# Performance work log

Hardware: AMD Instinct MI355X
Metric: run time of the kernel (lower is better)

Reference implementation:

```python
import jax, jax.numpy as jnp
import numpy as np


def fps(xyz, nsamples):
    # xyz: [B, N, 3] -> [B, nsamples] furthest-point-sample indices (int32)
    def single(p):
        N = p.shape[0]
        def step(carry, _):
            dists, last = carry
            d = jnp.sum((p - p[last]) ** 2, axis=-1)
            dists = jnp.minimum(dists, d)
            return (dists, jnp.argmax(dists).astype(jnp.int32)), last
        init = (jnp.full((N,), 1e10, p.dtype), jnp.int32(0))
        _, idx = jax.lax.scan(step, init, None, length=nsamples)
        return idx
    return jax.vmap(single)(xyz)


def bn_relu(x, g, b, m, v):
    # inference BatchNorm2d folded into scale/shift, then ReLU; x: [B,C,S,N]
    s = g * jax.lax.rsqrt(v + 1e-5)
    return jax.nn.relu(x * s[None, :, None, None] + (b - m * s)[None, :, None, None])


def setup_inputs() -> dict:
    key = jax.random.key(0)
    ks = jax.random.split(key, 6)
    B, N, C, S = 8, 16384, 64, 5
    return dict(
        fg_xyz=jax.random.normal(ks[0], (B, N, 3), jnp.float32),
        fg_features=jax.random.normal(ks[1], (B, C, N), jnp.float32),
        bg_xyz=jax.random.normal(ks[2], (B, N, 3), jnp.float32),
        bg_features=jax.random.normal(ks[3], (B, C, N), jnp.float32),
        w1=jax.random.normal(ks[4], (C, 2 * C), jnp.float32) * (1.0 / np.sqrt(2 * C)),
        g1=jnp.ones((C,), jnp.float32), b1=jnp.zeros((C,), jnp.float32),
        m1=jnp.zeros((C,), jnp.float32), v1=jnp.ones((C,), jnp.float32),
        w2=jax.random.normal(ks[5], (C, C), jnp.float32) * (1.0 / np.sqrt(C)),
        g2=jnp.ones((C,), jnp.float32), b2=jnp.zeros((C,), jnp.float32),
        m2=jnp.zeros((C,), jnp.float32), v2=jnp.ones((C,), jnp.float32),
        nsamples=5,
    )


def reference(fg_xyz, fg_features, bg_xyz, bg_features,
              w1, g1, b1, m1, v1, w2, g2, b2, m2, v2, nsamples):
    B, C, N = fg_features.shape
    S = nsamples
    # D-FPS sample S background points, gather their features: [B, C, S]
    idx = fps(bg_xyz, S)
    sample_bg = jnp.take_along_axis(
        bg_features, jnp.broadcast_to(idx[:, None, :], (B, C, S)), axis=2)
    fg_exp = fg_features[:, :, None, :]                           # [B, C, 1, N]
    # candidates = [fg itself, S sampled bg feats tiled over the N fg points]
    fused_origin = jnp.concatenate(
        [fg_exp, jnp.broadcast_to(sample_bg[:, :, :, None], (B, C, S, N))], axis=2)  # [B,C,S+1,N]
    # weight-net input: fg feature concatenated with each candidate along channels
    fusion_in = jnp.concatenate(
        [jnp.broadcast_to(fg_exp, (B, C, S + 1, N)), fused_origin], axis=1)          # [B,2C,S+1,N]
    h = bn_relu(jnp.einsum('oc,bcsn->bosn', w1, fusion_in), g1, b1, m1, v1)
    w = bn_relu(jnp.einsum('oc,bcsn->bosn', w2, h), g2, b2, m2, v2)                  # [B,C,S+1,N]
    final_feats = jnp.sum(w * fused_origin, axis=2, keepdims=True)                   # [B,C,1,N]
    return fg_xyz, final_feats
```

## Files before the change

### kernel.cpp

```cpp
#include <hip/hip_runtime.h>
#include <hip/hip_bf16.h>

#define B_ 8
#define N_ 16384
#define C_ 64
#define S_ 5

typedef float v4f __attribute__((ext_vector_type(4)));
typedef __bf16 v8bf __attribute__((ext_vector_type(8)));
typedef unsigned int v4u __attribute__((ext_vector_type(4)));

static __device__ __forceinline__ unsigned short f2bf(float f) {
    unsigned int u = __float_as_uint(f);
    u += 0x7fffu + ((u >> 16) & 1u);
    return (unsigned short)(u >> 16);
}
static __device__ __forceinline__ float bf2f(unsigned short s) {
    return __uint_as_float(((unsigned int)s) << 16);
}
static __device__ __forceinline__ unsigned int pk2bf(float a, float b) {
    float2 f2; f2.x = a; f2.y = b;
    __hip_bfloat162 h2 = __float22bfloat162_rn(f2);
    unsigned int u; __builtin_memcpy(&u, &h2, 4);
    return u;
}

__global__ __launch_bounds__(1024) void prep_all(
    const float* __restrict__ bg_xyz, const float* __restrict__ bg_feat,
    const float* __restrict__ w1, const float* __restrict__ g1, const float* __restrict__ b1,
    const float* __restrict__ m1, const float* __restrict__ v1,
    const float* __restrict__ w2, const float* __restrict__ g2, const float* __restrict__ b2,
    const float* __restrict__ m2, const float* __restrict__ v2,
    const float* __restrict__ fg_xyz, float* __restrict__ out_xyz,
    float* __restrict__ bb1, float* __restrict__ bb2,
    unsigned short* __restrict__ wa_bf, unsigned short* __restrict__ wc_bf,
    unsigned short* __restrict__ w2_bf,
    float* __restrict__ sbg, float* __restrict__ ebb) {
    const int blk = blockIdx.x;
    const int t = threadIdx.x;

    if (blk >= 9) {
        const int i = (blk - 9) * 1024 + t;
        ((float4*)out_xyz)[i] = ((const float4*)fg_xyz)[i];
        return;
    }

    if (blk == 8) {
        for (int i = t; i < 64 * 64; i += 1024) {
            const int o = i >> 6, c = i & 63;
            const float s1 = g1[o] / sqrtf(v1[o] + 1e-5f);
            const float s2 = g2[o] / sqrtf(v2[o] + 1e-5f);
            const float a = s1 * w1[o * 128 + c];
            const float bbv = s1 * w1[o * 128 + 64 + c];
            wa_bf[o * 64 + c] = f2bf(a);
            wc_bf[o * 64 + c] = f2bf(a + bbv);
            w2_bf[o * 64 + c] = f2bf(s2 * w2[o * 64 + c]);
        }
        if (t < 64) {
            const float s1 = g1[t] / sqrtf(v1[t] + 1e-5f);
            const float s2 = g2[t] / sqrtf(v2[t] + 1e-5f);
            bb1[t] = b1[t] - m1[t] * s1;
            bb2[t] = b2[t] - m2[t] * s2;
        }
        return;
    }

    const int b = blk;
    const float* p = bg_xyz + (size_t)b * N_ * 3;

    float px[16], py[16], pz[16], dist[16];
    {
        const float4* pv = (const float4*)p + t * 12;
#pragma unroll
        for (int g = 0; g < 4; ++g) {
            float4 a = pv[g * 3 + 0];
            float4 bq = pv[g * 3 + 1];
            float4 c = pv[g * 3 + 2];
            px[g * 4 + 0] = a.x;  py[g * 4 + 0] = a.y;  pz[g * 4 + 0] = a.z;
            px[g * 4 + 1] = a.w;  py[g * 4 + 1] = bq.x; pz[g * 4 + 1] = bq.y;
            px[g * 4 + 2] = bq.z; py[g * 4 + 2] = bq.w; pz[g * 4 + 2] = c.x;
            px[g * 4 + 3] = c.y;  py[g * 4 + 3] = c.z;  pz[g * 4 + 3] = c.w;
            dist[g * 4 + 0] = 1e10f; dist[g * 4 + 1] = 1e10f;
            dist[g * 4 + 2] = 1e10f; dist[g * 4 + 3] = 1e10f;
        }
    }

    __shared__ float s_best[16];
    __shared__ int s_bidx[16];
    __shared__ int s_last;
    __shared__ int s_idx[S_];
    __shared__ float sf[S_][64];
    int last = 0;
    if (t == 0) s_idx[0] = 0;

    for (int step = 1; step < S_; ++step) {
        const float lx = p[last * 3 + 0];
        const float ly = p[last * 3 + 1];
        const float lz = p[last * 3 + 2];
        float best = -1.0f;
        int bidx = 0;
#pragma unroll
        for (int k = 0; k < 16; ++k) {
            float dx = px[k] - lx, dy = py[k] - ly, dz = pz[k] - lz;
            float d = dx * dx + dy * dy + dz * dz;
            float nd = fminf(dist[k], d);
            dist[k] = nd;
            if (nd > best) { best = nd; bidx = t * 16 + k; }
        }
#pragma unroll
        for (int off = 32; off > 0; off >>= 1) {
            float ob = __shfl_down(best, off, 64);
            int oi = __shfl_down(bidx, off, 64);
            if (ob > best || (ob == best && oi < bidx)) { best = ob; bidx = oi; }
        }
        if ((t & 63) == 0) { s_best[t >> 6] = best; s_bidx[t >> 6] = bidx; }
        __syncthreads();
        if (t == 0) {
            float bb = s_best[0];
            int bi = s_bidx[0];
#pragma unroll
            for (int w = 1; w < 16; ++w) {
                if (s_best[w] > bb || (s_best[w] == bb && s_bidx[w] < bi)) {
                    bb = s_best[w];
                    bi = s_bidx[w];
                }
            }
            s_last = bi;
            s_idx[step] = bi;
        }
        __syncthreads();
        last = s_last;
        __syncthreads();
    }

    __syncthreads();
    if (t < S_ * 64) {
        const int j = t >> 6, c = t & 63;
        sf[j][c] = bg_feat[(size_t)b * C_ * N_ + (size_t)c * N_ + s_idx[j]];
    }
    __syncthreads();
    if (t < S_ * 64) {
        const int j = t >> 6, o = t & 63;
        const float s1 = g1[o] * rsqrtf(v1[o] + 1e-5f);
        const float4* wr = (const float4*)&w1[o * 128 + 64];
        float acc = 0.f;
#pragma unroll
        for (int c4 = 0; c4 < 16; ++c4) {
            float4 wv = wr[c4];
            acc += wv.x * sf[j][c4 * 4 + 0] + wv.y * sf[j][c4 * 4 + 1] +
                   wv.z * sf[j][c4 * 4 + 2] + wv.w * sf[j][c4 * 4 + 3];
        }
        sbg[(b * S_ + j) * 64 + o] = sf[j][o];
        ebb[(b * S_ + j) * 64 + o] = s1 * acc + (b1[o] - m1[o] * s1);
    }
}

#define PITCH 72

__global__ __launch_bounds__(256) void fusion_main(
    const float* __restrict__ fg_feat,
    const unsigned short* __restrict__ wa_bf, const unsigned short* __restrict__ wc_bf,
    const unsigned short* __restrict__ w2_bf,
    const float* __restrict__ bb1g, const float* __restrict__ bb2g,
    const float* __restrict__ ebbg, const float* __restrict__ sbgg,
    float* __restrict__ out) {
    __shared__ __align__(16) unsigned short Ft[64 * PITCH];
    __shared__ __align__(16) unsigned short Ht[2][64 * PITCH];
    __shared__ __align__(16) float cEbb[S_ * 64];
    __shared__ __align__(16) float cSbg[S_ * 64];
    __shared__ __align__(16) float cBb1[64];
    __shared__ __align__(16) float cBb2[64];

    const int t = threadIdx.x;
    const int b = blockIdx.y;
    const int n0 = blockIdx.x * 64;
    const float* Fg = fg_feat + (size_t)b * C_ * N_ + n0;

    {
        const int n = t & 63;
        const int cg = (t >> 6) * 16;
        float fr[16];
#pragma unroll
        for (int i = 0; i < 16; ++i) fr[i] = Fg[(size_t)(cg + i) * N_ + n];
        v4u w0, w1v;
#pragma unroll
        for (int i = 0; i < 8; ++i) {
            unsigned int pk = pk2bf(fr[2 * i], fr[2 * i + 1]);
            if (i < 4) w0[i] = pk; else w1v[i - 4] = pk;
        }
        *(v4u*)&Ft[n * PITCH + cg] = w0;
        *(v4u*)&Ft[n * PITCH + cg + 8] = w1v;
    }
    for (int i = t; i < S_ * 64; i += 256) {
        cEbb[i] = ebbg[b * (S_ * 64) + i];
        cSbg[i] = sbgg[b * (S_ * 64) + i];
    }
    if (t < 64) { cBb1[t] = bb1g[t]; cBb2[t] = bb2g[t]; }

    const int lane = t & 63;
    const int wv = t >> 6;
    const int o0 = wv * 16;
    const int m = lane & 15;
    const int q = lane >> 4;
    const int o4 = o0 + 4 * q;

    const int arow = o0 + m;
    v8bf aWa[2], aWc[2], aW2[2];
#pragma unroll
    for (int ks = 0; ks < 2; ++ks) {
        aWa[ks] = *(const v8bf*)&wa_bf[arow * 64 + ks * 32 + q * 8];
        aWc[ks] = *(const v8bf*)&wc_bf[arow * 64 + ks * 32 + q * 8];
        aW2[ks] = *(const v8bf*)&w2_bf[arow * 64 + ks * 32 + q * 8];
    }

    __syncthreads();

    v8bf bF[4][2];
#pragma unroll
    for (int nb = 0; nb < 4; ++nb)
#pragma unroll
        for (int ks = 0; ks < 2; ++ks)
            bF[nb][ks] = *(const v8bf*)&Ft[(nb * 16 + m) * PITCH + ks * 32 + q * 8];

    v4f U[4], U0[4];
#pragma unroll
    for (int nb = 0; nb < 4; ++nb) {
        v4f z = {0.f, 0.f, 0.f, 0.f};
        z = __builtin_amdgcn_mfma_f32_16x16x32_bf16(aWa[0], bF[nb][0], z, 0, 0, 0);
        U[nb] = __builtin_amdgcn_mfma_f32_16x16x32_bf16(aWa[1], bF[nb][1], z, 0, 0, 0);
        v4f z2 = {0.f, 0.f, 0.f, 0.f};
        z2 = __builtin_amdgcn_mfma_f32_16x16x32_bf16(aWc[0], bF[nb][0], z2, 0, 0, 0);
        U0[nb] = __builtin_amdgcn_mfma_f32_16x16x32_bf16(aWc[1], bF[nb][1], z2, 0, 0, 0);
    }

    v4f acc[4];
#pragma unroll
    for (int nb = 0; nb < 4; ++nb) acc[nb] = (v4f){0.f, 0.f, 0.f, 0.f};

    const v4f bb2r = *(const v4f*)&cBb2[o4];

#pragma unroll
    for (int s = 0; s < 6; ++s) {
        unsigned short* h = &Ht[s & 1][0];
        v4f cv = (s == 0) ? *(const v4f*)&cBb1[o4]
                          : *(const v4f*)&cEbb[(s - 1) * 64 + o4];
#pragma unroll
        for (int nb = 0; nb < 4; ++nb) {
            v4f u = (s == 0) ? U0[nb] : U[nb];
            unsigned int lo = pk2bf(fmaxf(u[0] + cv[0], 0.f), fmaxf(u[1] + cv[1], 0.f));
            unsigned int hi = pk2bf(fmaxf(u[2] + cv[2], 0.f), fmaxf(u[3] + cv[3], 0.f));
            unsigned long long vv = (unsigned long long)lo | ((unsigned long long)hi << 32);
            *(unsigned long long*)&h[(nb * 16 + m) * PITCH + o4] = vv;
        }
        __syncthreads();

#pragma unroll
        for (int nb = 0; nb < 4; ++nb) {
            v8bf h0 = *(const v8bf*)&h[(nb * 16 + m) * PITCH + q * 8];
            v8bf h1 = *(const v8bf*)&h[(nb * 16 + m) * PITCH + 32 + q * 8];
            v4f z = {0.f, 0.f, 0.f, 0.f};
            z = __builtin_amdgcn_mfma_f32_16x16x32_bf16(aW2[0], h0, z, 0, 0, 0);
            v4f p4 = __builtin_amdgcn_mfma_f32_16x16x32_bf16(aW2[1], h1, z, 0, 0, 0);

            if (s == 0) {
                unsigned long long fv =
                    *(const unsigned long long*)&Ft[(nb * 16 + m) * PITCH + o4];
#pragma unroll
                for (int r = 0; r < 4; ++r) {
                    float wgt = fmaxf(p4[r] + bb2r[r], 0.f);
                    acc[nb][r] += wgt * bf2f((unsigned short)(fv >> (16 * r)));
                }
            } else {
                const v4f sb = *(const v4f*)&cSbg[(s - 1) * 64 + o4];
#pragma unroll
                for (int r = 0; r < 4; ++r) {
                    float wgt = fmaxf(p4[r] + bb2r[r], 0.f);
                    acc[nb][r] += wgt * sb[r];
                }
            }
        }
    }

    const size_t outb = (size_t)b * C_ * N_ + n0;
#pragma unroll
    for (int nb = 0; nb < 4; ++nb)
#pragma unroll
        for (int r = 0; r < 4; ++r)
            out[outb + (size_t)(o4 + r) * N_ + (nb * 16 + m)] = acc[nb][r];
}

extern "C" void kernel_launch(void* const* d_in, const int* in_sizes, int n_in,
                              void* d_out, int out_size, void* d_ws, size_t ws_size,
                              hipStream_t stream) {
    const float* fg_xyz = (const float*)d_in[0];
    const float* fg_feat = (const float*)d_in[1];
    const float* bg_xyz = (const float*)d_in[2];
    const float* bg_feat = (const float*)d_in[3];
    const float* w1 = (const float*)d_in[4];
    const float* g1 = (const float*)d_in[5];
    const float* b1 = (const float*)d_in[6];
    const float* m1 = (const float*)d_in[7];
    const float* v1 = (const float*)d_in[8];
    const float* w2 = (const float*)d_in[9];
    const float* g2 = (const float*)d_in[10];
    const float* b2 = (const float*)d_in[11];
    const float* m2 = (const float*)d_in[12];
    const float* v2 = (const float*)d_in[13];

    float* ws = (float*)d_ws;
    float* ebb = ws;
    float* sbg = ebb + 2560;
    float* bb1 = sbg + 2560;
    float* bb2 = bb1 + 64;
    unsigned short* wa_bf = (unsigned short*)(bb2 + 64);
    unsigned short* wc_bf = wa_bf + 4096;
    unsigned short* w2_bf = wc_bf + 4096;

    float* out_feats = (float*)d_out + (size_t)B_ * N_ * 3;

    prep_all<<<105, 1024, 0, stream>>>(bg_xyz, bg_feat,
                                       w1, g1, b1, m1, v1, w2, g2, b2, m2, v2,
                                       fg_xyz, (float*)d_out,
                                       bb1, bb2, wa_bf, wc_bf, w2_bf, sbg, ebb);
    fusion_main<<<dim3(N_ / 64, B_), 256, 0, stream>>>(
        fg_feat, wa_bf, wc_bf, w2_bf, bb1, bb2, ebb, sbg, out_feats);
}
```

Before: 164.7 us.

## Fold weight prep and xyz copy into fusion kernel, two tiles per block with prefetch

```diff
diff --git a/kernel.cpp b/kernel.cpp
--- a/kernel.cpp
+++ b/kernel.cpp
@@ -10,62 +10,27 @@
 typedef __bf16 v8bf __attribute__((ext_vector_type(8)));
 typedef unsigned int v4u __attribute__((ext_vector_type(4)));
 
-static __device__ __forceinline__ unsigned short f2bf(float f) {
-    unsigned int u = __float_as_uint(f);
-    u += 0x7fffu + ((u >> 16) & 1u);
-    return (unsigned short)(u >> 16);
-}
-static __device__ __forceinline__ float bf2f(unsigned short s) {
-    return __uint_as_float(((unsigned int)s) << 16);
-}
 static __device__ __forceinline__ unsigned int pk2bf(float a, float b) {
     float2 f2; f2.x = a; f2.y = b;
     __hip_bfloat162 h2 = __float22bfloat162_rn(f2);
     unsigned int u; __builtin_memcpy(&u, &h2, 4);
     return u;
 }
-
-__global__ __launch_bounds__(1024) void prep_all(
+static __device__ __forceinline__ float bf2f(unsigned short s) {
+    return __uint_as_float(((unsigned int)s) << 16);
+}
+static __device__ __forceinline__ float getv(const v4f* h, int e) {
+    return e < 4 ? h[0][e] : h[1][e - 4];
+}
+
+__global__ __launch_bounds__(1024) void fps_sbg(
     const float* __restrict__ bg_xyz, const float* __restrict__ bg_feat,
-    const float* __restrict__ w1, const float* __restrict__ g1, const float* __restrict__ b1,
-    const float* __restrict__ m1, const float* __restrict__ v1,
-    const float* __restrict__ w2, const float* __restrict__ g2, const float* __restrict__ b2,
-    const float* __restrict__ m2, const float* __restrict__ v2,
-    const float* __restrict__ fg_xyz, float* __restrict__ out_xyz,
-    float* __restrict__ bb1, float* __restrict__ bb2,
-    unsigned short* __restrict__ wa_bf, unsigned short* __restrict__ wc_bf,
-    unsigned short* __restrict__ w2_bf,
+    const float* __restrict__ w1, const float* __restrict__ g1,
+    const float* __restrict__ b1, const float* __restrict__ m1,
+    const float* __restrict__ v1,
     float* __restrict__ sbg, float* __restrict__ ebb) {
-    const int blk = blockIdx.x;
+    const int b = blockIdx.x;
     const int t = threadIdx.x;
-
-    if (blk >= 9) {
-        const int i = (blk - 9) * 1024 + t;
-        ((float4*)out_xyz)[i] = ((const float4*)fg_xyz)[i];
-        return;
-    }
-
-    if (blk == 8) {
-        for (int i = t; i < 64 * 64; i += 1024) {
-            const int o = i >> 6, c = i & 63;
-            const float s1 = g1[o] / sqrtf(v1[o] + 1e-5f);
-            const float s2 = g2[o] / sqrtf(v2[o] + 1e-5f);
-            const float a = s1 * w1[o * 128 + c];
-            const float bbv = s1 * w1[o * 128 + 64 + c];
-            wa_bf[o * 64 + c] = f2bf(a);
-            wc_bf[o * 64 + c] = f2bf(a + bbv);
-            w2_bf[o * 64 + c] = f2bf(s2 * w2[o * 64 + c]);
-        }
-        if (t < 64) {
-            const float s1 = g1[t] / sqrtf(v1[t] + 1e-5f);
-            const float s2 = g2[t] / sqrtf(v2[t] + 1e-5f);
-            bb1[t] = b1[t] - m1[t] * s1;
-            bb2[t] = b2[t] - m2[t] * s2;
-        }
-        return;
-    }
-
-    const int b = blk;
     const float* p = bg_xyz + (size_t)b * N_ * 3;
 
     float px[16], py[16], pz[16], dist[16];
@@ -133,7 +98,6 @@
         __syncthreads();
     }
 
-    __syncthreads();
     if (t < S_ * 64) {
         const int j = t >> 6, c = t & 63;
         sf[j][c] = bg_feat[(size_t)b * C_ * N_ + (size_t)c * N_ + s_idx[j]];
@@ -158,13 +122,16 @@
 #define PITCH 72
 
 __global__ __launch_bounds__(256) void fusion_main(
-    const float* __restrict__ fg_feat,
-    const unsigned short* __restrict__ wa_bf, const unsigned short* __restrict__ wc_bf,
-    const unsigned short* __restrict__ w2_bf,
-    const float* __restrict__ bb1g, const float* __restrict__ bb2g,
+    const float* __restrict__ fg_xyz, const float* __restrict__ fg_feat,
+    const float* __restrict__ w1, const float* __restrict__ g1,
+    const float* __restrict__ b1, const float* __restrict__ m1,
+    const float* __restrict__ v1,
+    const float* __restrict__ w2, const float* __restrict__ g2,
+    const float* __restrict__ b2, const float* __restrict__ m2,
+    const float* __restrict__ v2,
     const float* __restrict__ ebbg, const float* __restrict__ sbgg,
-    float* __restrict__ out) {
-    __shared__ __align__(16) unsigned short Ft[64 * PITCH];
+    float* __restrict__ out_xyz, float* __restrict__ out) {
+    __shared__ __align__(16) unsigned short Ft[2][64 * PITCH];
     __shared__ __align__(16) unsigned short Ht[2][64 * PITCH];
     __shared__ __align__(16) float cEbb[S_ * 64];
     __shared__ __align__(16) float cSbg[S_ * 64];
@@ -172,30 +139,20 @@
     __shared__ __align__(16) float cBb2[64];
 
     const int t = threadIdx.x;
-    const int b = blockIdx.y;
-    const int n0 = blockIdx.x * 64;
-    const float* Fg = fg_feat + (size_t)b * C_ * N_ + n0;
-
-    {
-        const int n = t & 63;
-        const int cg = (t >> 6) * 16;
-        float fr[16];
-#pragma unroll
-        for (int i = 0; i < 16; ++i) fr[i] = Fg[(size_t)(cg + i) * N_ + n];
-        v4u w0, w1v;
-#pragma unroll
-        for (int i = 0; i < 8; ++i) {
-            unsigned int pk = pk2bf(fr[2 * i], fr[2 * i + 1]);
-            if (i < 4) w0[i] = pk; else w1v[i - 4] = pk;
-        }
-        *(v4u*)&Ft[n * PITCH + cg] = w0;
-        *(v4u*)&Ft[n * PITCH + cg + 8] = w1v;
-    }
-    for (int i = t; i < S_ * 64; i += 256) {
-        cEbb[i] = ebbg[b * (S_ * 64) + i];
-        cSbg[i] = sbgg[b * (S_ * 64) + i];
-    }
-    if (t < 64) { cBb1[t] = bb1g[t]; cBb2[t] = bb2g[t]; }
+    const int bid = blockIdx.x;
+
+    if (bid >= 1024) {
+        const int base = (bid - 1024) * 1024 + t;
+#pragma unroll
+        for (int k = 0; k < 4; ++k)
+            ((float4*)out_xyz)[base + k * 256] = ((const float4*)fg_xyz)[base + k * 256];
+        return;
+    }
+
+    const int b = bid >> 7;
+    const int nx = bid & 127;
+    const float* Fbase = fg_feat + (size_t)b * C_ * N_;
+    const size_t outb = (size_t)b * C_ * N_;
 
     const int lane = t & 63;
     const int wv = t >> 6;
@@ -203,90 +160,168 @@
     const int m = lane & 15;
     const int q = lane >> 4;
     const int o4 = o0 + 4 * q;
-
     const int arow = o0 + m;
+
+    const int sn = t & 63;
+    const int cg = (t >> 6) * 16;
+
+    {
+        const float* Fg = Fbase + (size_t)nx * 64 + sn;
+        float fr[16];
+#pragma unroll
+        for (int i = 0; i < 16; ++i) fr[i] = Fg[(size_t)(cg + i) * N_];
+        v4u w0, w1v;
+#pragma unroll
+        for (int i = 0; i < 8; ++i) {
+            unsigned int pk = pk2bf(fr[2 * i], fr[2 * i + 1]);
+            if (i < 4) w0[i] = pk; else w1v[i - 4] = pk;
+        }
+        *(v4u*)&Ft[0][sn * PITCH + cg] = w0;
+        *(v4u*)&Ft[0][sn * PITCH + cg + 8] = w1v;
+    }
+
     v8bf aWa[2], aWc[2], aW2[2];
-#pragma unroll
-    for (int ks = 0; ks < 2; ++ks) {
-        aWa[ks] = *(const v8bf*)&wa_bf[arow * 64 + ks * 32 + q * 8];
-        aWc[ks] = *(const v8bf*)&wc_bf[arow * 64 + ks * 32 + q * 8];
-        aW2[ks] = *(const v8bf*)&w2_bf[arow * 64 + ks * 32 + q * 8];
+    {
+        const float s1 = g1[arow] * rsqrtf(v1[arow] + 1e-5f);
+        const float s2 = g2[arow] * rsqrtf(v2[arow] + 1e-5f);
+        const float* w1r = w1 + arow * 128;
+        const float* w2r = w2 + arow * 64;
+#pragma unroll
+        for (int ks = 0; ks < 2; ++ks) {
+            const int k0 = ks * 32 + q * 8;
+            v4f wA[2], wB[2], w2v[2];
+            wA[0] = *(const v4f*)&w1r[k0];
+            wA[1] = *(const v4f*)&w1r[k0 + 4];
+            wB[0] = *(const v4f*)&w1r[64 + k0];
+            wB[1] = *(const v4f*)&w1r[64 + k0 + 4];
+            w2v[0] = *(const v4f*)&w2r[k0];
+            w2v[1] = *(const v4f*)&w2r[k0 + 4];
+            unsigned int ua[4], uc[4], u2[4];
+#pragma unroll
+            for (int d = 0; d < 4; ++d) {
+                float a0 = getv(wA, 2 * d), a1 = getv(wA, 2 * d + 1);
+                float b0 = getv(wB, 2 * d), b1v = getv(wB, 2 * d + 1);
+                float c0 = getv(w2v, 2 * d), c1 = getv(w2v, 2 * d + 1);
+                ua[d] = pk2bf(s1 * a0, s1 * a1);
+                uc[d] = pk2bf(s1 * (a0 + b0), s1 * (a1 + b1v));
+                u2[d] = pk2bf(s2 * c0, s2 * c1);
+            }
+            __builtin_memcpy(&aWa[ks], ua, 16);
+            __builtin_memcpy(&aWc[ks], uc, 16);
+            __builtin_memcpy(&aW2[ks], u2, 16);
+        }
+    }
+
+    for (int i = t; i < S_ * 64; i += 256) {
+        cEbb[i] = ebbg[b * (S_ * 64) + i];
+        cSbg[i] = sbgg[b * (S_ * 64) + i];
+    }
+    if (t < 64) {
+        const float s1 = g1[t] * rsqrtf(v1[t] + 1e-5f);
+        const float s2 = g2[t] * rsqrtf(v2[t] + 1e-5f);
+        cBb1[t] = b1[t] - m1[t] * s1;
+        cBb2[t] = b2[t] - m2[t] * s2;
     }
 
     __syncthreads();
 
-    v8bf bF[4][2];
-#pragma unroll
-    for (int nb = 0; nb < 4; ++nb)
-#pragma unroll
-        for (int ks = 0; ks < 2; ++ks)
-            bF[nb][ks] = *(const v8bf*)&Ft[(nb * 16 + m) * PITCH + ks * 32 + q * 8];
-
-    v4f U[4], U0[4];
-#pragma unroll
-    for (int nb = 0; nb < 4; ++nb) {
-        v4f z = {0.f, 0.f, 0.f, 0.f};
-        z = __builtin_amdgcn_mfma_f32_16x16x32_bf16(aWa[0], bF[nb][0], z, 0, 0, 0);
-        U[nb] = __builtin_amdgcn_mfma_f32_16x16x32_bf16(aWa[1], bF[nb][1], z, 0, 0, 0);
-        v4f z2 = {0.f, 0.f, 0.f, 0.f};
-        z2 = __builtin_amdgcn_mfma_f32_16x16x32_bf16(aWc[0], bF[nb][0], z2, 0, 0, 0);
-        U0[nb] = __builtin_amdgcn_mfma_f32_16x16x32_bf16(aWc[1], bF[nb][1], z2, 0, 0, 0);
-    }
-
-    v4f acc[4];
-#pragma unroll
-    for (int nb = 0; nb < 4; ++nb) acc[nb] = (v4f){0.f, 0.f, 0.f, 0.f};
+    float fr1[16];
+    {
+        const float* Fg1 = Fbase + (size_t)(nx + 128) * 64 + sn;
+#pragma unroll
+        for (int i = 0; i < 16; ++i) fr1[i] = Fg1[(size_t)(cg + i) * N_];
+    }
 
     const v4f bb2r = *(const v4f*)&cBb2[o4];
 
-#pragma unroll
-    for (int s = 0; s < 6; ++s) {
-        unsigned short* h = &Ht[s & 1][0];
-        v4f cv = (s == 0) ? *(const v4f*)&cBb1[o4]
-                          : *(const v4f*)&cEbb[(s - 1) * 64 + o4];
+    auto tile_compute = [&](const unsigned short* F, size_t obase) {
+        v8bf bF[4][2];
+#pragma unroll
+        for (int nb = 0; nb < 4; ++nb)
+#pragma unroll
+            for (int ks = 0; ks < 2; ++ks)
+                bF[nb][ks] = *(const v8bf*)&F[(nb * 16 + m) * PITCH + ks * 32 + q * 8];
+
+        v4f U[4], U0[4];
 #pragma unroll
         for (int nb = 0; nb < 4; ++nb) {
-            v4f u = (s == 0) ? U0[nb] : U[nb];
-            unsigned int lo = pk2bf(fmaxf(u[0] + cv[0], 0.f), fmaxf(u[1] + cv[1], 0.f));
-            unsigned int hi = pk2bf(fmaxf(u[2] + cv[2], 0.f), fmaxf(u[3] + cv[3], 0.f));
-            unsigned long long vv = (unsigned long long)lo | ((unsigned long long)hi << 32);
-            *(unsigned long long*)&h[(nb * 16 + m) * PITCH + o4] = vv;
-        }
-        __syncthreads();
-
-#pragma unroll
-        for (int nb = 0; nb < 4; ++nb) {
-            v8bf h0 = *(const v8bf*)&h[(nb * 16 + m) * PITCH + q * 8];
-            v8bf h1 = *(const v8bf*)&h[(nb * 16 + m) * PITCH + 32 + q * 8];
             v4f z = {0.f, 0.f, 0.f, 0.f};
-            z = __builtin_amdgcn_mfma_f32_16x16x32_bf16(aW2[0], h0, z, 0, 0, 0);
-            v4f p4 = __builtin_amdgcn_mfma_f32_16x16x32_bf16(aW2[1], h1, z, 0, 0, 0);
-
-            if (s == 0) {
-                unsigned long long fv =
-                    *(const unsigned long long*)&Ft[(nb * 16 + m) * PITCH + o4];
-#pragma unroll
-                for (int r = 0; r < 4; ++r) {
-                    float wgt = fmaxf(p4[r] + bb2r[r], 0.f);
-                    acc[nb][r] += wgt * bf2f((unsigned short)(fv >> (16 * r)));
-                }
-            } else {
-                const v4f sb = *(const v4f*)&cSbg[(s - 1) * 64 + o4];
-#pragma unroll
-                for (int r = 0; r < 4; ++r) {
-                    float wgt = fmaxf(p4[r] + bb2r[r], 0.f);
-                    acc[nb][r] += wgt * sb[r];
+            z = __builtin_amdgcn_mfma_f32_16x16x32_bf16(aWa[0], bF[nb][0], z, 0, 0, 0);
+            U[nb] = __builtin_amdgcn_mfma_f32_16x16x32_bf16(aWa[1], bF[nb][1], z, 0, 0, 0);
+            v4f z2 = {0.f, 0.f, 0.f, 0.f};
+            z2 = __builtin_amdgcn_mfma_f32_16x16x32_bf16(aWc[0], bF[nb][0], z2, 0, 0, 0);
+            U0[nb] = __builtin_amdgcn_mfma_f32_16x16x32_bf16(aWc[1], bF[nb][1], z2, 0, 0, 0);
+        }
+
+        v4f acc[4];
+#pragma unroll
+        for (int nb = 0; nb < 4; ++nb) acc[nb] = (v4f){0.f, 0.f, 0.f, 0.f};
+
+#pragma unroll
+        for (int s = 0; s < 6; ++s) {
+            unsigned short* h = &Ht[s & 1][0];
+            v4f cv = (s == 0) ? *(const v4f*)&cBb1[o4]
+                              : *(const v4f*)&cEbb[(s - 1) * 64 + o4];
+#pragma unroll
+            for (int nb = 0; nb < 4; ++nb) {
+                v4f u = (s == 0) ? U0[nb] : U[nb];
+                unsigned int lo = pk2bf(fmaxf(u[0] + cv[0], 0.f), fmaxf(u[1] + cv[1], 0.f));
+                unsigned int hi = pk2bf(fmaxf(u[2] + cv[2], 0.f), fmaxf(u[3] + cv[3], 0.f));
+                unsigned long long vv = (unsigned long long)lo | ((unsigned long long)hi << 32);
+                *(unsigned long long*)&h[(nb * 16 + m) * PITCH + o4] = vv;
+            }
+            __syncthreads();
+
+            v4f sb;
+            if (s > 0) sb = *(const v4f*)&cSbg[(s - 1) * 64 + o4];
+#pragma unroll
+            for (int nb = 0; nb < 4; ++nb) {
+                v8bf h0 = *(const v8bf*)&h[(nb * 16 + m) * PITCH + q * 8];
+                v8bf h1 = *(const v8bf*)&h[(nb * 16 + m) * PITCH + 32 + q * 8];
+                v4f z = {0.f, 0.f, 0.f, 0.f};
+                z = __builtin_amdgcn_mfma_f32_16x16x32_bf16(aW2[0], h0, z, 0, 0, 0);
+                v4f p4 = __builtin_amdgcn_mfma_f32_16x16x32_bf16(aW2[1], h1, z, 0, 0, 0);
+
+                if (s == 0) {
+                    unsigned long long fv =
+                        *(const unsigned long long*)&F[(nb * 16 + m) * PITCH + o4];
+#pragma unroll
+                    for (int r = 0; r < 4; ++r) {
+                        float wgt = fmaxf(p4[r] + bb2r[r], 0.f);
+                        acc[nb][r] += wgt * bf2f((unsigned short)(fv >> (16 * r)));
+                    }
+                } else {
+#pragma unroll
+                    for (int r = 0; r < 4; ++r) {
+                        float wgt = fmaxf(p4[r] + bb2r[r], 0.f);
+                        acc[nb][r] += wgt * sb[r];
+                    }
                 }
             }
         }
-    }
-
-    const size_t outb = (size_t)b * C_ * N_ + n0;
-#pragma unroll
-    for (int nb = 0; nb < 4; ++nb)
-#pragma unroll
-        for (int r = 0; r < 4; ++r)
-            out[outb + (size_t)(o4 + r) * N_ + (nb * 16 + m)] = acc[nb][r];
+
+#pragma unroll
+        for (int nb = 0; nb < 4; ++nb)
+#pragma unroll
+            for (int r = 0; r < 4; ++r)
+                out[obase + (size_t)(o4 + r) * N_ + (nb * 16 + m)] = acc[nb][r];
+    };
+
+    tile_compute(&Ft[0][0], outb + (size_t)nx * 64);
+
+    {
+        v4u w0, w1v;
+#pragma unroll
+        for (int i = 0; i < 8; ++i) {
+            unsigned int pk = pk2bf(fr1[2 * i], fr1[2 * i + 1]);
+            if (i < 4) w0[i] = pk; else w1v[i - 4] = pk;
+        }
+        *(v4u*)&Ft[1][sn * PITCH + cg] = w0;
+        *(v4u*)&Ft[1][sn * PITCH + cg + 8] = w1v;
+    }
+    __syncthreads();
+
+    tile_compute(&Ft[1][0], outb + (size_t)(nx + 128) * 64);
 }
 
 extern "C" void kernel_launch(void* const* d_in, const int* in_sizes, int n_in,
@@ -310,18 +345,12 @@
     float* ws = (float*)d_ws;
     float* ebb = ws;
     float* sbg = ebb + 2560;
-    float* bb1 = sbg + 2560;
-    float* bb2 = bb1 + 64;
-    unsigned short* wa_bf = (unsigned short*)(bb2 + 64);
-    unsigned short* wc_bf = wa_bf + 4096;
-    unsigned short* w2_bf = wc_bf + 4096;
 
     float* out_feats = (float*)d_out + (size_t)B_ * N_ * 3;
 
-    prep_all<<<105, 1024, 0, stream>>>(bg_xyz, bg_feat,
-                                       w1, g1, b1, m1, v1, w2, g2, b2, m2, v2,
-                                       fg_xyz, (float*)d_out,
-                                       bb1, bb2, wa_bf, wc_bf, w2_bf, sbg, ebb);
-    fusion_main<<<dim3(N_ / 64, B_), 256, 0, stream>>>(
-        fg_feat, wa_bf, wc_bf, w2_bf, bb1, bb2, ebb, sbg, out_feats);
-}
+    fps_sbg<<<B_, 1024, 0, stream>>>(bg_xyz, bg_feat, w1, g1, b1, m1, v1,
+                                     sbg, ebb);
+    fusion_main<<<1120, 256, 0, stream>>>(
+        fg_xyz, fg_feat, w1, g1, b1, m1, v1, w2, g2, b2, m2, v2,
+        ebb, sbg, (float*)d_out, out_feats);
+}
```

New measurement: 168.6 us. +2.3%, slower.
